# Performance work log

Measured on AMD Instinct MI355X. Metric: run time of the kernel, lower is better.

## Reference

```python
import jax, jax.numpy as jnp
import numpy as np
import math

H, NH, NKV, HD, FF = 1024, 16, 4, 64, 4096
B, S = 2, 2048
EPS, THETA = 1e-6, 10000.0


def _rmsnorm(x, w, eps=EPS):
    v = jnp.mean(x.astype(jnp.float32) ** 2, axis=-1, keepdims=True)
    return (x.astype(jnp.float32) * jax.lax.rsqrt(v + eps)).astype(x.dtype) * w


def _rope_tables(seq_len, head_dim, theta=THETA):
    inv_freq = 1.0 / (theta ** (jnp.arange(0, head_dim, 2, dtype=jnp.float32) / head_dim))
    freqs = jnp.arange(seq_len, dtype=jnp.float32)[:, None] * inv_freq[None, :]
    emb = jnp.concatenate([freqs, freqs], axis=-1)  # [S, HD]
    return jnp.cos(emb), jnp.sin(emb)


def _rotate_half(x):
    x1, x2 = jnp.split(x, 2, axis=-1)
    return jnp.concatenate([-x2, x1], axis=-1)


def _apply_rope(x, cos, sin):
    # x: [B, h, S, HD]; cos/sin: [S, HD] broadcast over batch/heads
    return x * cos[None, None] + _rotate_half(x) * sin[None, None]


def setup_inputs() -> dict:
    key = jax.random.key(0)
    ks = jax.random.split(key, 12)
    std = 0.02
    return {
        "hidden_states": jax.random.normal(ks[0], (B, S, H), jnp.float32),
        "kv_states": jax.random.normal(ks[1], (B, S, H), jnp.float32),
        "attention_mask": jnp.zeros((B, 1, S, S), jnp.float32),
        "ln1_w": jnp.ones((H,), jnp.float32),
        "ln2_w": jnp.ones((H,), jnp.float32),
        "Wq": jax.random.normal(ks[2], (H, NH * HD), jnp.float32) * std,
        "Wk": jax.random.normal(ks[3], (H, NKV * HD), jnp.float32) * std,
        "Wv": jax.random.normal(ks[4], (H, NKV * HD), jnp.float32) * std,
        "Wo": jax.random.normal(ks[5], (NH * HD, H), jnp.float32) * std,
        "Wgate": jax.random.normal(ks[6], (H, FF), jnp.float32) * std,
        "Wup": jax.random.normal(ks[7], (H, FF), jnp.float32) * std,
        "Wdown": jax.random.normal(ks[8], (FF, H), jnp.float32) * std,
    }


def reference(hidden_states, kv_states, attention_mask, ln1_w, ln2_w,
              Wq, Wk, Wv, Wo, Wgate, Wup, Wdown):
    bsz, q_len, _ = hidden_states.shape
    k_len = kv_states.shape[1]

    residual = hidden_states
    h = _rmsnorm(hidden_states, ln1_w)   # input_layernorm on queries
    kv = _rmsnorm(kv_states, ln1_w)      # same norm applied to kv_states

    q = (h @ Wq).reshape(bsz, q_len, NH, HD).transpose(0, 2, 1, 3)    # [B,NH,Sq,HD]
    k = (kv @ Wk).reshape(bsz, k_len, NKV, HD).transpose(0, 2, 1, 3)  # [B,NKV,Sk,HD]
    v = (kv @ Wv).reshape(bsz, k_len, NKV, HD).transpose(0, 2, 1, 3)

    cos_q, sin_q = _rope_tables(q_len, HD)
    cos_k, sin_k = _rope_tables(k_len, HD)
    q = _apply_rope(q, cos_q, sin_q)
    k = _apply_rope(k, cos_k, sin_k)

    # repeat_kv: GQA expand to NH heads
    groups = NH // NKV
    k = jnp.repeat(k, groups, axis=1)
    v = jnp.repeat(v, groups, axis=1)

    scores = jnp.einsum("bhqd,bhkd->bhqk", q, k) / math.sqrt(HD)
    scores = scores + attention_mask  # additive mask [B,1,Sq,Sk]
    probs = jax.nn.softmax(scores.astype(jnp.float32), axis=-1).astype(q.dtype)
    attn = jnp.einsum("bhqk,bhkd->bhqd", probs, v)
    attn = attn.transpose(0, 2, 1, 3).reshape(bsz, q_len, NH * HD)
    attn = attn @ Wo

    hidden = residual + attn

    residual = hidden
    x = _rmsnorm(hidden, ln2_w)
    x = (jax.nn.silu(x @ Wgate) * (x @ Wup)) @ Wdown  # SwiGLU MLP
    return residual + x
```

## Files before the change

### kernel.cpp

```cpp
#include <hip/hip_runtime.h>
#include <math.h>

#define SS 2048

typedef __attribute__((ext_vector_type(8))) short s16x8;
typedef __attribute__((ext_vector_type(4))) float f32x4;

__device__ __forceinline__ unsigned short f2bf(float f) {
  union { float f; unsigned u; } a; a.f = f;
  unsigned r = a.u + 0x7fffu + ((a.u >> 16) & 1u);
  return (unsigned short)(r >> 16);
}
__device__ __forceinline__ float bf2f(unsigned short b) {
  union { unsigned u; float f; } a; a.u = ((unsigned)b) << 16;
  return a.f;
}
__device__ __forceinline__ unsigned short cvt1(float f) {
  unsigned v;
  asm("v_cvt_pk_bf16_f32 %0, %1, %1" : "=v"(v) : "v"(f));
  return (unsigned short)v;
}
__device__ __forceinline__ float fexp2(float x) {
  float r; asm("v_exp_f32 %0, %1" : "=v"(r) : "v"(x)); return r;
}
__device__ __forceinline__ void async16(void* lds, const void* g) {
  __builtin_amdgcn_global_load_lds(
      (const __attribute__((address_space(1))) unsigned int*)g,
      (__attribute__((address_space(3))) unsigned int*)lds, 16, 0, 0);
}
__device__ __forceinline__ f32x4 mfma_bf16(s16x8 a, s16x8 b, f32x4 c) {
  return __builtin_amdgcn_mfma_f32_16x16x32_bf16(a, b, c, 0, 0, 0);
}

template <int CTRL>
__device__ __forceinline__ float fdpp(float x) {
  union { float f; int i; } a; a.f = x;
  a.i = __builtin_amdgcn_update_dpp(0, a.i, CTRL, 0xF, 0xF, true);
  return a.f;
}
__device__ __forceinline__ float red16max(float x) {
  x = fmaxf(x, fdpp<0xB1>(x));
  x = fmaxf(x, fdpp<0x4E>(x));
  x = fmaxf(x, fdpp<0x141>(x));
  x = fmaxf(x, fdpp<0x140>(x));
  return x;
}

__global__ __launch_bounds__(256) void k_transpose(const float* __restrict__ W,
                                                   unsigned short* __restrict__ WT,
                                                   int K, int N) {
  __shared__ float tile[32][33];
  int t = threadIdx.x;
  int tx = t & 31, ty = t >> 5;
  int n0 = blockIdx.x * 32, k0 = blockIdx.y * 32;
#pragma unroll
  for (int i = 0; i < 4; ++i)
    tile[ty + 8 * i][tx] = W[(size_t)(k0 + ty + 8 * i) * N + n0 + tx];
  __syncthreads();
#pragma unroll
  for (int i = 0; i < 4; ++i)
    WT[(size_t)(n0 + ty + 8 * i) * K + k0 + tx] = f2bf(tile[tx][ty + 8 * i]);
}

__global__ __launch_bounds__(256) void k_vtrans(const unsigned short* __restrict__ QKV,
                                                unsigned short* __restrict__ VT) {
  __shared__ unsigned short tile[32][33];
  int t = threadIdx.x, tx = t & 31, ty = t >> 5;
  int s0 = blockIdx.x * 32, d0 = blockIdx.y * 32;
  int bk = blockIdx.z; int b = bk >> 2, kvh = bk & 3;
#pragma unroll
  for (int i = 0; i < 4; ++i)
    tile[ty + 8 * i][tx] =
        QKV[((size_t)b * SS + s0 + ty + 8 * i) * 1536 + 1280 + kvh * 64 + d0 + tx];
  __syncthreads();
#pragma unroll
  for (int i = 0; i < 4; ++i)
    VT[((size_t)bk * 64 + d0 + ty + 8 * i) * SS + s0 + tx] = tile[tx][ty + 8 * i];
}

__global__ void k_rope_tables(float* __restrict__ cosT, float* __restrict__ sinT) {
  int idx = blockIdx.x * 256 + threadIdx.x;
  int s = idx >> 5, i = idx & 31;
  double ang = (double)s * pow(10000.0, -(double)(2 * i) / 64.0);
  cosT[idx] = (float)cos(ang);
  sinT[idx] = (float)sin(ang);
}

__global__ __launch_bounds__(256) void k_rmsnorm(const float* __restrict__ X,
                                                 const float* __restrict__ Wt,
                                                 unsigned short* __restrict__ Y) {
  int row = blockIdx.x, t = threadIdx.x;
  float4 v = ((const float4*)X)[(size_t)row * 256 + t];
  float ssq = v.x * v.x + v.y * v.y + v.z * v.z + v.w * v.w;
#pragma unroll
  for (int m = 1; m < 64; m <<= 1) ssq += __shfl_xor(ssq, m);
  __shared__ float red[4];
  if ((t & 63) == 0) red[t >> 6] = ssq;
  __syncthreads();
  float sc = rsqrtf((red[0] + red[1] + red[2] + red[3]) * (1.0f / 1024.0f) + 1e-6f);
  float4 wv = ((const float4*)Wt)[t];
  ushort4 o;
  o.x = f2bf(v.x * sc * wv.x); o.y = f2bf(v.y * sc * wv.y);
  o.z = f2bf(v.z * sc * wv.z); o.w = f2bf(v.w * sc * wv.w);
  ((ushort4*)Y)[(size_t)row * 256 + t] = o;
}

__global__ __launch_bounds__(256) void k_rope(unsigned short* __restrict__ X,
                                              const float* __restrict__ cosT,
                                              const float* __restrict__ sinT,
                                              int stride) {
  int idx = blockIdx.x * 256 + threadIdx.x;
  int seg = idx & 7, tok = idx >> 3;
  int head = blockIdx.y;
  int s = tok & (SS - 1);
  int d0 = seg * 4;
  unsigned short* p = X + (size_t)tok * stride + head * 64;
  ushort4 lo = *(ushort4*)&p[d0];
  ushort4 hi = *(ushort4*)&p[d0 + 32];
  float4 cs = *(const float4*)&cosT[s * 32 + d0];
  float4 sn = *(const float4*)&sinT[s * 32 + d0];
  ushort4 olo, ohi;
  olo.x = f2bf(bf2f(lo.x) * cs.x - bf2f(hi.x) * sn.x);
  olo.y = f2bf(bf2f(lo.y) * cs.y - bf2f(hi.y) * sn.y);
  olo.z = f2bf(bf2f(lo.z) * cs.z - bf2f(hi.z) * sn.z);
  olo.w = f2bf(bf2f(lo.w) * cs.w - bf2f(hi.w) * sn.w);
  ohi.x = f2bf(bf2f(hi.x) * cs.x + bf2f(lo.x) * sn.x);
  ohi.y = f2bf(bf2f(hi.y) * cs.y + bf2f(lo.y) * sn.y);
  ohi.z = f2bf(bf2f(hi.z) * cs.z + bf2f(lo.z) * sn.z);
  ohi.w = f2bf(bf2f(hi.w) * cs.w + bf2f(lo.w) * sn.w);
  *(ushort4*)&p[d0] = olo;
  *(ushort4*)&p[d0 + 32] = ohi;
}

template <int EPI, int BN>
__global__ __launch_bounds__(256) void k_gemm(const unsigned short* __restrict__ A,
                                              const unsigned short* __restrict__ BT,
                                              int K, int ldc,
                                              unsigned short* Cb,
                                              float* __restrict__ Cf,
                                              const float* __restrict__ Res) {
  constexpr int NW = BN / 32;
  __shared__ __align__(16) unsigned short at[128 * 32];
  __shared__ __align__(16) unsigned short bt[BN * 32];
  int t = threadIdx.x, w = t >> 6, l = t & 63;
  int g = l >> 4, c = l & 15;
  int wm = w >> 1, wn = w & 1;
  f32x4 acc[4][NW] = {};
  const unsigned short* gA = A + (size_t)(blockIdx.y * 128 + (t >> 2)) * K + (t & 3) * 8;
  const unsigned short* gB = BT + (size_t)(blockIdx.x * BN + (t >> 2)) * K + (t & 3) * 8;
  unsigned short* dA = &at[w * 512];
  unsigned short* dB = &bt[w * 512];
  const int nk = K >> 5;
  for (int kt = 0; kt < nk; ++kt) {
    async16(dA, gA);
    async16(dA + 2048, gA + (size_t)64 * K);
    async16(dB, gB);
    if (BN == 128) async16(dB + 2048, gB + (size_t)64 * K);
    gA += 32; gB += 32;
    __syncthreads();
    s16x8 af[4], bfr[NW];
#pragma unroll
    for (int m = 0; m < 4; ++m) af[m] = *(const s16x8*)&at[(wm * 64 + m * 16 + c) * 32 + g * 8];
#pragma unroll
    for (int n = 0; n < NW; ++n)
      bfr[n] = *(const s16x8*)&bt[(wn * (BN / 2) + n * 16 + c) * 32 + g * 8];
#pragma unroll
    for (int m = 0; m < 4; ++m)
#pragma unroll
      for (int n = 0; n < NW; ++n)
        acc[m][n] = mfma_bf16(af[m], bfr[n], acc[m][n]);
    __syncthreads();
  }
  size_t rb = (size_t)blockIdx.y * 128 + wm * 64;
  size_t cbase = (size_t)blockIdx.x * BN + wn * (BN / 2);
#pragma unroll
  for (int m = 0; m < 4; ++m)
#pragma unroll
    for (int n = 0; n < NW; ++n)
#pragma unroll
      for (int r = 0; r < 4; ++r) {
        size_t row = rb + m * 16 + g * 4 + r;
        size_t col = cbase + n * 16 + c;
        float v = acc[m][n][r];
        if (EPI == 0) Cb[row * ldc + col] = f2bf(v);
        else Cf[row * ldc + col] = v + Res[row * ldc + col];
      }
}

__global__ __launch_bounds__(256) void k_gateup(const unsigned short* __restrict__ A,
                                                const unsigned short* __restrict__ BTg,
                                                const unsigned short* __restrict__ BTu,
                                                unsigned short* __restrict__ Cb) {
  __shared__ __align__(16) unsigned short at[128 * 32];
  __shared__ __align__(16) unsigned short bg[64 * 32];
  __shared__ __align__(16) unsigned short bu[64 * 32];
  int t = threadIdx.x, w = t >> 6, l = t & 63;
  int g = l >> 4, c = l & 15;
  int wm = w >> 1, wn = w & 1;
  f32x4 ag[4][2] = {}, au[4][2] = {};
  const unsigned short* gA = A + (size_t)(blockIdx.y * 128 + (t >> 2)) * 1024 + (t & 3) * 8;
  const unsigned short* gG = BTg + (size_t)(blockIdx.x * 64 + (t >> 2)) * 1024 + (t & 3) * 8;
  const unsigned short* gU = BTu + (size_t)(blockIdx.x * 64 + (t >> 2)) * 1024 + (t & 3) * 8;
  unsigned short* dA = &at[w * 512];
  unsigned short* dG = &bg[w * 512];
  unsigned short* dU = &bu[w * 512];
  for (int kt = 0; kt < 32; ++kt) {
    async16(dA, gA);
    async16(dA + 2048, gA + (size_t)64 * 1024);
    async16(dG, gG);
    async16(dU, gU);
    gA += 32; gG += 32; gU += 32;
    __syncthreads();
    s16x8 af[4], bgf[2], buf_[2];
#pragma unroll
    for (int m = 0; m < 4; ++m) af[m] = *(const s16x8*)&at[(wm * 64 + m * 16 + c) * 32 + g * 8];
#pragma unroll
    for (int n = 0; n < 2; ++n) {
      bgf[n] = *(const s16x8*)&bg[(wn * 32 + n * 16 + c) * 32 + g * 8];
      buf_[n] = *(const s16x8*)&bu[(wn * 32 + n * 16 + c) * 32 + g * 8];
    }
#pragma unroll
    for (int m = 0; m < 4; ++m)
#pragma unroll
      for (int n = 0; n < 2; ++n) {
        ag[m][n] = mfma_bf16(af[m], bgf[n], ag[m][n]);
        au[m][n] = mfma_bf16(af[m], buf_[n], au[m][n]);
      }
    __syncthreads();
  }
  size_t rb = (size_t)blockIdx.y * 128 + wm * 64;
  size_t cb = (size_t)blockIdx.x * 64 + wn * 32;
#pragma unroll
  for (int m = 0; m < 4; ++m)
#pragma unroll
    for (int n = 0; n < 2; ++n)
#pragma unroll
      for (int r = 0; r < 4; ++r) {
        size_t row = rb + m * 16 + g * 4 + r;
        size_t col = cb + n * 16 + c;
        float gv = ag[m][n][r], uv = au[m][n][r];
        Cb[row * 4096 + col] = f2bf(gv / (1.0f + __expf(-gv)) * uv);
      }
}

__global__ __launch_bounds__(512) void k_attn(const unsigned short* __restrict__ Q,
                                              const unsigned short* __restrict__ K,
                                              const unsigned short* __restrict__ VT,
                                              const float* __restrict__ mask,
                                              unsigned short* __restrict__ Out) {
  __shared__ __align__(16) unsigned short Ks[2][64 * 64];
  __shared__ __align__(16) unsigned short VTs[2][64 * 64];
  __shared__ __align__(16) unsigned short Ps[8 * 16 * 68];
  const float LOG2E = 1.44269504f;
  const float SCL2 = 0.125f * 1.44269504f;
  int t = threadIdx.x, w = t >> 6, l = t & 63;
  int g = l >> 4, c = l & 15;
  int qw = w >> 2, hh = w & 3;
  int blk = blockIdx.x;
  int qt = blk & 63, kvh = (blk >> 6) & 3, b = blk >> 8;
  size_t tokQ = (size_t)b * SS + qt * 32 + qw * 16;
  int head = kvh * 4 + hh;
  s16x8 qf[2];
#pragma unroll
  for (int st = 0; st < 2; ++st)
    qf[st] = *(const s16x8*)&Q[(tokQ + c) * 1536 + head * 64 + st * 32 + g * 8];
  const s16x8 one8 = {(short)0x3F80, (short)0x3F80, (short)0x3F80, (short)0x3F80,
                      (short)0x3F80, (short)0x3F80, (short)0x3F80, (short)0x3F80};

  int srow = t >> 3;
  int soff = srow * 64 + (((t & 7) ^ (srow & 7)) << 3);
  const unsigned short* gK = K + ((size_t)b * SS + srow) * 1536 + kvh * 64 + (t & 7) * 8;
  const unsigned short* gV = VT + ((size_t)(b * 4 + kvh) * 64 + srow) * SS + (t & 7) * 8;

  int4 rK = *(const int4*)gK;
  int4 rV = *(const int4*)gV;
  *(int4*)&Ks[0][soff] = rK;
  *(int4*)&VTs[0][soff] = rV;

  const float* mrow = mask + (size_t)b * SS * SS + (size_t)(qt * 32 + qw * 16 + g * 4) * SS + c;
  float mcur[4][4], mnxt[4][4];
#pragma unroll
  for (int n = 0; n < 4; ++n)
#pragma unroll
    for (int r = 0; r < 4; ++r) mcur[n][r] = mrow[(size_t)r * SS + n * 16] * LOG2E;

  f32x4 aco[4] = {};
  f32x4 acl = {};
  float mrun[4];
#pragma unroll
  for (int r = 0; r < 4; ++r) mrun[r] = -1e30f;
  unsigned short* myP = &Ps[w * (16 * 68)];
  __syncthreads();

  for (int kt = 0; kt < 32; ++kt) {
    const unsigned short* Kc = Ks[kt & 1];
    const unsigned short* Vc = VTs[kt & 1];
    int nx = kt < 31 ? kt + 1 : 31;
    rK = *(const int4*)(gK + (size_t)nx * 64 * 1536);
    rV = *(const int4*)(gV + nx * 64);
#pragma unroll
    for (int n = 0; n < 4; ++n)
#pragma unroll
      for (int r = 0; r < 4; ++r) mnxt[n][r] = mrow[(size_t)r * SS + nx * 64 + n * 16];

    f32x4 as[4] = {};
    __builtin_amdgcn_s_setprio(1);
#pragma unroll
    for (int st = 0; st < 2; ++st)
#pragma unroll
      for (int n = 0; n < 4; ++n) {
        s16x8 kb = *(const s16x8*)&Kc[(n * 16 + c) * 64 + (((st * 4 + g) ^ (c & 7)) << 3)];
        as[n] = mfma_bf16(qf[st], kb, as[n]);
      }
    __builtin_amdgcn_s_setprio(0);
    float sv[4][4];
#pragma unroll
    for (int n = 0; n < 4; ++n)
#pragma unroll
      for (int r = 0; r < 4; ++r) sv[n][r] = as[n][r] * SCL2 + mcur[n][r];
    float mx[4];
#pragma unroll
    for (int r = 0; r < 4; ++r) {
      float m0 = fmaxf(fmaxf(sv[0][r], sv[1][r]), fmaxf(sv[2][r], sv[3][r]));
      mx[r] = red16max(m0);
    }
    float need = fmaxf(fmaxf(mx[0] - mrun[0], mx[1] - mrun[1]),
                       fmaxf(mx[2] - mrun[2], mx[3] - mrun[3]));
    if (__any(need > 8.0f)) {
#pragma unroll
      for (int r = 0; r < 4; ++r) {
        float mnew = fmaxf(mrun[r], mx[r]);
        float alpha = fexp2(mrun[r] - mnew);
        acl[r] *= alpha;
#pragma unroll
        for (int n = 0; n < 4; ++n) aco[n][r] *= alpha;
        mrun[r] = mnew;
      }
    }
#pragma unroll
    for (int r = 0; r < 4; ++r)
#pragma unroll
      for (int n = 0; n < 4; ++n)
        myP[(g * 4 + r) * 68 + n * 16 + c] = cvt1(fexp2(sv[n][r] - mrun[r]));
    asm volatile("s_waitcnt lgkmcnt(0)" ::: "memory");
    __builtin_amdgcn_sched_barrier(0);
    __builtin_amdgcn_s_setprio(1);
#pragma unroll
    for (int st = 0; st < 2; ++st) {
      s16x8 pa = *(const s16x8*)&myP[c * 68 + st * 32 + g * 8];
#pragma unroll
      for (int n = 0; n < 4; ++n) {
        s16x8 vb = *(const s16x8*)&Vc[(n * 16 + c) * 64 + (((st * 4 + g) ^ (c & 7)) << 3)];
        aco[n] = mfma_bf16(pa, vb, aco[n]);
      }
      acl = mfma_bf16(pa, one8, acl);
    }
    __builtin_amdgcn_s_setprio(0);
    if (kt < 31) {
      *(int4*)&Ks[(kt + 1) & 1][soff] = rK;
      *(int4*)&VTs[(kt + 1) & 1][soff] = rV;
    }
#pragma unroll
    for (int n = 0; n < 4; ++n)
#pragma unroll
      for (int r = 0; r < 4; ++r) mcur[n][r] = mnxt[n][r] * LOG2E;
    __syncthreads();
  }
#pragma unroll
  for (int n = 0; n < 4; ++n)
#pragma unroll
    for (int r = 0; r < 4; ++r) {
      float v = aco[n][r] / acl[r];
      Out[(tokQ + g * 4 + r) * 1024 + head * 64 + n * 16 + c] = f2bf(v);
    }
}

extern "C" void kernel_launch(void* const* d_in, const int* in_sizes, int n_in,
                              void* d_out, int out_size, void* d_ws, size_t ws_size,
                              hipStream_t stream) {
  (void)in_sizes; (void)n_in; (void)out_size; (void)ws_size;
  const float* hidden = (const float*)d_in[0];
  const float* kvst   = (const float*)d_in[1];
  const float* maskp  = (const float*)d_in[2];
  const float* ln1    = (const float*)d_in[3];
  const float* ln2    = (const float*)d_in[4];
  const float* Wq     = (const float*)d_in[5];
  const float* Wk     = (const float*)d_in[6];
  const float* Wv     = (const float*)d_in[7];
  const float* Wo     = (const float*)d_in[8];
  const float* Wg     = (const float*)d_in[9];
  const float* Wu     = (const float*)d_in[10];
  const float* Wd     = (const float*)d_in[11];
  float* out = (float*)d_out;

  char* ws = (char*)d_ws;
  size_t off = 0;
  auto alloc = [&](size_t bytes) { char* p = ws + off; off += (bytes + 255) & ~(size_t)255; return p; };
  unsigned short* WTqkv = (unsigned short*)alloc((size_t)1536 * 1024 * 2);
  unsigned short* WTo   = (unsigned short*)alloc((size_t)1024 * 1024 * 2);
  unsigned short* WTg   = (unsigned short*)alloc((size_t)4096 * 1024 * 2);
  unsigned short* WTu   = (unsigned short*)alloc((size_t)4096 * 1024 * 2);
  unsigned short* WTd   = (unsigned short*)alloc((size_t)1024 * 4096 * 2);
  float* cosT           = (float*)alloc((size_t)2048 * 32 * 4);
  float* sinT           = (float*)alloc((size_t)2048 * 32 * 4);
  unsigned short* hn    = (unsigned short*)alloc((size_t)4096 * 1024 * 2);
  unsigned short* kvn   = (unsigned short*)alloc((size_t)4096 * 1024 * 2);
  unsigned short* QKVb  = (unsigned short*)alloc((size_t)4096 * 1536 * 2);
  unsigned short* VTg   = (unsigned short*)alloc((size_t)8 * 64 * SS * 2);
  float* hid2           = (float*)alloc((size_t)4096 * 1024 * 4);
  unsigned short* inter = (unsigned short*)alloc((size_t)4096 * 4096 * 2);
  unsigned short* attnb = hn;
  unsigned short* h2n   = kvn;

  k_transpose<<<dim3(32, 32), 256, 0, stream>>>(Wq, WTqkv, 1024, 1024);
  k_transpose<<<dim3(8, 32), 256, 0, stream>>>(Wk, WTqkv + (size_t)1024 * 1024, 1024, 256);
  k_transpose<<<dim3(8, 32), 256, 0, stream>>>(Wv, WTqkv + (size_t)1280 * 1024, 1024, 256);
  k_transpose<<<dim3(32, 32), 256, 0, stream>>>(Wo, WTo, 1024, 1024);
  k_transpose<<<dim3(128, 32), 256, 0, stream>>>(Wg, WTg, 1024, 4096);
  k_transpose<<<dim3(128, 32), 256, 0, stream>>>(Wu, WTu, 1024, 4096);
  k_transpose<<<dim3(32, 128), 256, 0, stream>>>(Wd, WTd, 4096, 1024);
  k_rope_tables<<<256, 256, 0, stream>>>(cosT, sinT);
  k_rmsnorm<<<4096, 256, 0, stream>>>(hidden, ln1, hn);
  k_rmsnorm<<<4096, 256, 0, stream>>>(kvst, ln1, kvn);
  k_gemm<0, 64><<<dim3(16, 32), 256, 0, stream>>>(hn, WTqkv, 1024, 1536, QKVb, nullptr, nullptr);
  k_gemm<0, 64><<<dim3(8, 32), 256, 0, stream>>>(kvn, WTqkv + (size_t)1024 * 1024, 1024, 1536,
                                                 QKVb + 1024, nullptr, nullptr);
  k_rope<<<dim3(128, 20), 256, 0, stream>>>(QKVb, cosT, sinT, 1536);
  k_vtrans<<<dim3(64, 2, 8), 256, 0, stream>>>(QKVb, VTg);
  k_attn<<<512, 512, 0, stream>>>(QKVb, QKVb + 1024, VTg, maskp, attnb);
  k_gemm<1, 64><<<dim3(16, 32), 256, 0, stream>>>(attnb, WTo, 1024, 1024, nullptr, hid2, hidden);
  k_rmsnorm<<<4096, 256, 0, stream>>>(hid2, ln2, h2n);
  k_gateup<<<dim3(64, 32), 256, 0, stream>>>(h2n, WTg, WTu, inter);
  k_gemm<1, 64><<<dim3(16, 32), 256, 0, stream>>>(inter, WTd, 4096, 1024, nullptr, out, hid2);
}
```

Baseline: 360.1 us.

## Rewrite attention with 32x32x16 MFMA, transposed scores, register-resident P

The attention kernel switches from 16x16x32 to 32x32x16 bf16 MFMA and computes S^T = K·Q^T, so each lane owns one query column. Probabilities are repacked into A-operand fragments with cross-half lane shuffles instead of a round trip through LDS, which removes the Ps buffer and its waitcnt barrier. Each wave now handles 32 queries for one head, and the block shrinks to 256 threads. The trade-offs are more accumulator registers per lane, alpha broadcast via shuffles during rescale, and a strided mask and output access pattern.

```diff
diff --git a/kernel.cpp b/kernel.cpp
--- a/kernel.cpp
+++ b/kernel.cpp
@@ -5,6 +5,7 @@
 
 typedef __attribute__((ext_vector_type(8))) short s16x8;
 typedef __attribute__((ext_vector_type(4))) float f32x4;
+typedef __attribute__((ext_vector_type(16))) float f32x16;
 
 __device__ __forceinline__ unsigned short f2bf(float f) {
   union { float f; unsigned u; } a; a.f = f;
@@ -15,10 +16,8 @@
   union { unsigned u; float f; } a; a.u = ((unsigned)b) << 16;
   return a.f;
 }
-__device__ __forceinline__ unsigned short cvt1(float f) {
-  unsigned v;
-  asm("v_cvt_pk_bf16_f32 %0, %1, %1" : "=v"(v) : "v"(f));
-  return (unsigned short)v;
+__device__ __forceinline__ unsigned cvtpk(float a, float b) {
+  unsigned d; asm("v_cvt_pk_bf16_f32 %0, %1, %2" : "=v"(d) : "v"(a), "v"(b)); return d;
 }
 __device__ __forceinline__ float fexp2(float x) {
   float r; asm("v_exp_f32 %0, %1" : "=v"(r) : "v"(x)); return r;
@@ -31,19 +30,8 @@
 __device__ __forceinline__ f32x4 mfma_bf16(s16x8 a, s16x8 b, f32x4 c) {
   return __builtin_amdgcn_mfma_f32_16x16x32_bf16(a, b, c, 0, 0, 0);
 }
-
-template <int CTRL>
-__device__ __forceinline__ float fdpp(float x) {
-  union { float f; int i; } a; a.f = x;
-  a.i = __builtin_amdgcn_update_dpp(0, a.i, CTRL, 0xF, 0xF, true);
-  return a.f;
-}
-__device__ __forceinline__ float red16max(float x) {
-  x = fmaxf(x, fdpp<0xB1>(x));
-  x = fmaxf(x, fdpp<0x4E>(x));
-  x = fmaxf(x, fdpp<0x141>(x));
-  x = fmaxf(x, fdpp<0x140>(x));
-  return x;
+__device__ __forceinline__ f32x16 mfma32(s16x8 a, s16x8 b, f32x16 c) {
+  return __builtin_amdgcn_mfma_f32_32x32x16_bf16(a, b, c, 0, 0, 0);
 }
 
 __global__ __launch_bounds__(256) void k_transpose(const float* __restrict__ W,
@@ -243,136 +231,161 @@
       }
 }
 
-__global__ __launch_bounds__(512) void k_attn(const unsigned short* __restrict__ Q,
+__global__ __launch_bounds__(256) void k_attn(const unsigned short* __restrict__ Q,
                                               const unsigned short* __restrict__ K,
                                               const unsigned short* __restrict__ VT,
                                               const float* __restrict__ mask,
                                               unsigned short* __restrict__ Out) {
   __shared__ __align__(16) unsigned short Ks[2][64 * 64];
   __shared__ __align__(16) unsigned short VTs[2][64 * 64];
-  __shared__ __align__(16) unsigned short Ps[8 * 16 * 68];
   const float LOG2E = 1.44269504f;
-  const float SCL2 = 0.125f * 1.44269504f;
   int t = threadIdx.x, w = t >> 6, l = t & 63;
-  int g = l >> 4, c = l & 15;
-  int qw = w >> 2, hh = w & 3;
+  int q32 = l & 31, hi = l >> 5;
   int blk = blockIdx.x;
   int qt = blk & 63, kvh = (blk >> 6) & 3, b = blk >> 8;
-  size_t tokQ = (size_t)b * SS + qt * 32 + qw * 16;
-  int head = kvh * 4 + hh;
-  s16x8 qf[2];
-#pragma unroll
-  for (int st = 0; st < 2; ++st)
-    qf[st] = *(const s16x8*)&Q[(tokQ + c) * 1536 + head * 64 + st * 32 + g * 8];
+  int head = kvh * 4 + w;
+  size_t tokQ = (size_t)b * SS + qt * 32;
+
+  s16x8 qfr[4];
+#pragma unroll
+  for (int d = 0; d < 4; ++d)
+    qfr[d] = *(const s16x8*)&Q[(tokQ + q32) * 1536 + head * 64 + d * 16 + hi * 8];
   const s16x8 one8 = {(short)0x3F80, (short)0x3F80, (short)0x3F80, (short)0x3F80,
                       (short)0x3F80, (short)0x3F80, (short)0x3F80, (short)0x3F80};
 
-  int srow = t >> 3;
-  int soff = srow * 64 + (((t & 7) ^ (srow & 7)) << 3);
-  const unsigned short* gK = K + ((size_t)b * SS + srow) * 1536 + kvh * 64 + (t & 7) * 8;
-  const unsigned short* gV = VT + ((size_t)(b * 4 + kvh) * 64 + srow) * SS + (t & 7) * 8;
-
-  int4 rK = *(const int4*)gK;
-  int4 rV = *(const int4*)gV;
-  *(int4*)&Ks[0][soff] = rK;
-  *(int4*)&VTs[0][soff] = rV;
-
-  const float* mrow = mask + (size_t)b * SS * SS + (size_t)(qt * 32 + qw * 16 + g * 4) * SS + c;
-  float mcur[4][4], mnxt[4][4];
-#pragma unroll
-  for (int n = 0; n < 4; ++n)
-#pragma unroll
-    for (int r = 0; r < 4; ++r) mcur[n][r] = mrow[(size_t)r * SS + n * 16] * LOG2E;
-
-  f32x4 aco[4] = {};
-  f32x4 acl = {};
-  float mrun[4];
-#pragma unroll
-  for (int r = 0; r < 4; ++r) mrun[r] = -1e30f;
-  unsigned short* myP = &Ps[w * (16 * 68)];
+  int id0 = t, id1 = t + 256;
+  int row0 = id0 >> 3, b80 = id0 & 7;
+  int row1 = id1 >> 3, b81 = id1 & 7;
+  int so0 = row0 * 64 + ((b80 ^ (row0 & 7)) << 3);
+  int so1 = row1 * 64 + ((b81 ^ (row1 & 7)) << 3);
+  const unsigned short* gK = K + (size_t)b * SS * 1536 + kvh * 64;
+  const unsigned short* gV = VT + (size_t)(b * 4 + kvh) * 64 * SS;
+
+  int4 rK0 = *(const int4*)(gK + (size_t)row0 * 1536 + b80 * 8);
+  int4 rK1 = *(const int4*)(gK + (size_t)row1 * 1536 + b81 * 8);
+  int4 rV0 = *(const int4*)(gV + (size_t)row0 * SS + b80 * 8);
+  int4 rV1 = *(const int4*)(gV + (size_t)row1 * SS + b81 * 8);
+  *(int4*)&Ks[0][so0] = rK0; *(int4*)&Ks[0][so1] = rK1;
+  *(int4*)&VTs[0][so0] = rV0; *(int4*)&VTs[0][so1] = rV1;
+
+  const float* mrowp = mask + (size_t)b * SS * SS + (size_t)(qt * 32 + q32) * SS + 4 * hi;
+  float mc0[16], mc1[16];
+#pragma unroll
+  for (int r = 0; r < 16; ++r) {
+    mc0[r] = mrowp[(r & 3) + 8 * (r >> 2)];
+    mc1[r] = mrowp[32 + (r & 3) + 8 * (r >> 2)];
+  }
+
+  f32x16 aco0 = {}, aco1 = {}, acl = {};
+  float mrun = -1e30f;
   __syncthreads();
 
   for (int kt = 0; kt < 32; ++kt) {
     const unsigned short* Kc = Ks[kt & 1];
     const unsigned short* Vc = VTs[kt & 1];
-    int nx = kt < 31 ? kt + 1 : 31;
-    rK = *(const int4*)(gK + (size_t)nx * 64 * 1536);
-    rV = *(const int4*)(gV + nx * 64);
-#pragma unroll
-    for (int n = 0; n < 4; ++n)
-#pragma unroll
-      for (int r = 0; r < 4; ++r) mnxt[n][r] = mrow[(size_t)r * SS + nx * 64 + n * 16];
-
-    f32x4 as[4] = {};
+    if (kt < 31) {
+      int kb = (kt + 1) * 64;
+      rK0 = *(const int4*)(gK + (size_t)(kb + row0) * 1536 + b80 * 8);
+      rK1 = *(const int4*)(gK + (size_t)(kb + row1) * 1536 + b81 * 8);
+      rV0 = *(const int4*)(gV + (size_t)row0 * SS + kb + b80 * 8);
+      rV1 = *(const int4*)(gV + (size_t)row1 * SS + kb + b81 * 8);
+    }
+    f32x16 s0 = {}, s1 = {};
     __builtin_amdgcn_s_setprio(1);
 #pragma unroll
-    for (int st = 0; st < 2; ++st)
-#pragma unroll
-      for (int n = 0; n < 4; ++n) {
-        s16x8 kb = *(const s16x8*)&Kc[(n * 16 + c) * 64 + (((st * 4 + g) ^ (c & 7)) << 3)];
-        as[n] = mfma_bf16(qf[st], kb, as[n]);
-      }
+    for (int d = 0; d < 4; ++d) {
+      s16x8 ka = *(const s16x8*)&Kc[q32 * 64 + (((d * 2 + hi) ^ (q32 & 7)) << 3)];
+      s0 = mfma32(ka, qfr[d], s0);
+      int r2 = 32 + q32;
+      s16x8 kb2 = *(const s16x8*)&Kc[r2 * 64 + (((d * 2 + hi) ^ (r2 & 7)) << 3)];
+      s1 = mfma32(kb2, qfr[d], s1);
+    }
     __builtin_amdgcn_s_setprio(0);
-    float sv[4][4];
-#pragma unroll
-    for (int n = 0; n < 4; ++n)
-#pragma unroll
-      for (int r = 0; r < 4; ++r) sv[n][r] = as[n][r] * SCL2 + mcur[n][r];
-    float mx[4];
-#pragma unroll
-    for (int r = 0; r < 4; ++r) {
-      float m0 = fmaxf(fmaxf(sv[0][r], sv[1][r]), fmaxf(sv[2][r], sv[3][r]));
-      mx[r] = red16max(m0);
-    }
-    float need = fmaxf(fmaxf(mx[0] - mrun[0], mx[1] - mrun[1]),
-                       fmaxf(mx[2] - mrun[2], mx[3] - mrun[3]));
-    if (__any(need > 8.0f)) {
-#pragma unroll
-      for (int r = 0; r < 4; ++r) {
-        float mnew = fmaxf(mrun[r], mx[r]);
-        float alpha = fexp2(mrun[r] - mnew);
-        acl[r] *= alpha;
-#pragma unroll
-        for (int n = 0; n < 4; ++n) aco[n][r] *= alpha;
-        mrun[r] = mnew;
-      }
-    }
-#pragma unroll
-    for (int r = 0; r < 4; ++r)
-#pragma unroll
-      for (int n = 0; n < 4; ++n)
-        myP[(g * 4 + r) * 68 + n * 16 + c] = cvt1(fexp2(sv[n][r] - mrun[r]));
-    asm volatile("s_waitcnt lgkmcnt(0)" ::: "memory");
-    __builtin_amdgcn_sched_barrier(0);
+    float sv0[16], sv1[16];
+#pragma unroll
+    for (int r = 0; r < 16; ++r) {
+      sv0[r] = (s0[r] * 0.125f + mc0[r]) * LOG2E;
+      sv1[r] = (s1[r] * 0.125f + mc1[r]) * LOG2E;
+    }
+    {
+      int nk = (kt < 31 ? kt + 1 : 31) * 64;
+#pragma unroll
+      for (int r = 0; r < 16; ++r) {
+        mc0[r] = mrowp[nk + (r & 3) + 8 * (r >> 2)];
+        mc1[r] = mrowp[nk + 32 + (r & 3) + 8 * (r >> 2)];
+      }
+    }
+    float mx = sv0[0];
+#pragma unroll
+    for (int r = 1; r < 16; ++r) mx = fmaxf(mx, sv0[r]);
+#pragma unroll
+    for (int r = 0; r < 16; ++r) mx = fmaxf(mx, sv1[r]);
+    mx = fmaxf(mx, __shfl_xor(mx, 32));
+    if (__any(mx > mrun + 8.0f)) {
+      float mnew = fmaxf(mrun, mx);
+      float alpha = fexp2(mrun - mnew);
+      mrun = mnew;
+#pragma unroll
+      for (int r = 0; r < 16; ++r) {
+        float al = __shfl(alpha, (r & 3) + 8 * (r >> 2) + 4 * hi);
+        aco0[r] *= al; aco1[r] *= al; acl[r] *= al;
+      }
+    }
+    s16x8 pa[4];
+#pragma unroll
+    for (int ks = 0; ks < 2; ++ks) {
+      float p[16];
+      if (ks == 0) {
+#pragma unroll
+        for (int r = 0; r < 16; ++r) p[r] = fexp2(sv0[r] - mrun);
+      } else {
+#pragma unroll
+        for (int r = 0; r < 16; ++r) p[r] = fexp2(sv1[r] - mrun);
+      }
+      unsigned w8[8];
+#pragma unroll
+      for (int i = 0; i < 8; ++i) w8[i] = cvtpk(p[2 * i], p[2 * i + 1]);
+      unsigned sd0 = hi ? w8[0] : w8[2];
+      unsigned sd1 = hi ? w8[1] : w8[3];
+      unsigned sd2 = hi ? w8[4] : w8[6];
+      unsigned sd3 = hi ? w8[5] : w8[7];
+      unsigned rc0 = (unsigned)__shfl_xor((int)sd0, 32);
+      unsigned rc1 = (unsigned)__shfl_xor((int)sd1, 32);
+      unsigned rc2 = (unsigned)__shfl_xor((int)sd2, 32);
+      unsigned rc3 = (unsigned)__shfl_xor((int)sd3, 32);
+      union { int4 i; s16x8 v; } fa, fb;
+      fa.i.x = hi ? rc0 : w8[0]; fa.i.y = hi ? rc1 : w8[1];
+      fa.i.z = hi ? w8[2] : rc0; fa.i.w = hi ? w8[3] : rc1;
+      fb.i.x = hi ? rc2 : w8[4]; fb.i.y = hi ? rc3 : w8[5];
+      fb.i.z = hi ? w8[6] : rc2; fb.i.w = hi ? w8[7] : rc3;
+      pa[2 * ks] = fa.v;
+      pa[2 * ks + 1] = fb.v;
+    }
     __builtin_amdgcn_s_setprio(1);
 #pragma unroll
-    for (int st = 0; st < 2; ++st) {
-      s16x8 pa = *(const s16x8*)&myP[c * 68 + st * 32 + g * 8];
-#pragma unroll
-      for (int n = 0; n < 4; ++n) {
-        s16x8 vb = *(const s16x8*)&Vc[(n * 16 + c) * 64 + (((st * 4 + g) ^ (c & 7)) << 3)];
-        aco[n] = mfma_bf16(pa, vb, aco[n]);
-      }
-      acl = mfma_bf16(pa, one8, acl);
+    for (int ks = 0; ks < 4; ++ks) {
+      s16x8 va = *(const s16x8*)&Vc[q32 * 64 + (((ks * 2 + hi) ^ (q32 & 7)) << 3)];
+      aco0 = mfma32(pa[ks], va, aco0);
+      int r2 = 32 + q32;
+      s16x8 vb2 = *(const s16x8*)&Vc[r2 * 64 + (((ks * 2 + hi) ^ (r2 & 7)) << 3)];
+      aco1 = mfma32(pa[ks], vb2, aco1);
+      acl = mfma32(pa[ks], one8, acl);
     }
     __builtin_amdgcn_s_setprio(0);
     if (kt < 31) {
-      *(int4*)&Ks[(kt + 1) & 1][soff] = rK;
-      *(int4*)&VTs[(kt + 1) & 1][soff] = rV;
-    }
-#pragma unroll
-    for (int n = 0; n < 4; ++n)
-#pragma unroll
-      for (int r = 0; r < 4; ++r) mcur[n][r] = mnxt[n][r] * LOG2E;
+      int nb = (kt + 1) & 1;
+      *(int4*)&Ks[nb][so0] = rK0; *(int4*)&Ks[nb][so1] = rK1;
+      *(int4*)&VTs[nb][so0] = rV0; *(int4*)&VTs[nb][so1] = rV1;
+    }
     __syncthreads();
   }
 #pragma unroll
-  for (int n = 0; n < 4; ++n)
-#pragma unroll
-    for (int r = 0; r < 4; ++r) {
-      float v = aco[n][r] / acl[r];
-      Out[(tokQ + g * 4 + r) * 1024 + head * 64 + n * 16 + c] = f2bf(v);
-    }
+  for (int r = 0; r < 16; ++r) {
+    float inv = 1.0f / acl[r];
+    size_t orow = tokQ + (r & 3) + 8 * (r >> 2) + 4 * hi;
+    Out[orow * 1024 + head * 64 + q32] = f2bf(aco0[r] * inv);
+    Out[orow * 1024 + head * 64 + 32 + q32] = f2bf(aco1[r] * inv);
+  }
 }
 
 extern "C" void kernel_launch(void* const* d_in, const int* in_sizes, int n_in,
@@ -427,7 +440,7 @@
                                                  QKVb + 1024, nullptr, nullptr);
   k_rope<<<dim3(128, 20), 256, 0, stream>>>(QKVb, cosT, sinT, 1536);
   k_vtrans<<<dim3(64, 2, 8), 256, 0, stream>>>(QKVb, VTg);
-  k_attn<<<512, 512, 0, stream>>>(QKVb, QKVb + 1024, VTg, maskp, attnb);
+  k_attn<<<512, 256, 0, stream>>>(QKVb, QKVb + 1024, VTg, maskp, attnb);
   k_gemm<1, 64><<<dim3(16, 32), 256, 0, stream>>>(attnb, WTo, 1024, 1024, nullptr, hid2, hidden);
   k_rmsnorm<<<4096, 256, 0, stream>>>(hid2, ln2, h2n);
   k_gateup<<<dim3(64, 32), 256, 0, stream>>>(h2n, WTg, WTu, inter);
```

Measured after the change: 345.9 us. -3.9%, faster.
